# Performance work log

Hardware: AMD Instinct MI355X
Metric: run time of the kernel (lower is better)

## Reference

```python
import jax, jax.numpy as jnp
import numpy as np

B, L, D_MODEL, H, MAX_DIST = 4, 1024, 1024, 16, 64
DEPTH = D_MODEL // H
VOCAB = 2 * MAX_DIST + 1


def setup_inputs() -> dict:
    key = jax.random.key(0)
    ks = jax.random.split(key, 12)
    s = 0.02
    return {
        "x": jax.random.normal(ks[0], (B, L, D_MODEL), jnp.float32),
        "mask": jnp.zeros((B, 1, 1, L), jnp.float32),
        "wq": jax.random.normal(ks[1], (D_MODEL, D_MODEL), jnp.float32) * s,
        "bq": jnp.zeros((D_MODEL,), jnp.float32),
        "wk": jax.random.normal(ks[2], (D_MODEL, D_MODEL), jnp.float32) * s,
        "bk": jnp.zeros((D_MODEL,), jnp.float32),
        "wv": jax.random.normal(ks[3], (D_MODEL, D_MODEL), jnp.float32) * s,
        "bv": jnp.zeros((D_MODEL,), jnp.float32),
        "wo": jax.random.normal(ks[4], (D_MODEL, D_MODEL), jnp.float32) * s,
        "bo": jnp.zeros((D_MODEL,), jnp.float32),
        "rel_k_table": jax.random.normal(ks[5], (VOCAB, DEPTH), jnp.float32) * s,
        "rel_v_table": jax.random.normal(ks[6], (VOCAB, DEPTH), jnp.float32) * s,
    }


def _split_heads(t):
    # [B, L, d_model] -> [B, H, L, depth]
    return t.reshape(B, L, H, DEPTH).transpose(0, 2, 1, 3)


def reference(x, mask, wq, bq, wk, bk, wv, bv, wo, bo, rel_k_table, rel_v_table):
    # q/k/v projections (self-attention)
    q = _split_heads(x @ wq + bq)
    k = _split_heads(x @ wk + bk)
    v = _split_heads(x @ wv + bv)

    # relative positions matrix [L, L], clipped to [-MAX_DIST, MAX_DIST] then shifted
    r = jnp.arange(L)
    rel_mat = jnp.clip(r[None, :] - r[:, None], -MAX_DIST, MAX_DIST) + MAX_DIST
    rel_k = rel_k_table[rel_mat]  # [L, L, depth]
    rel_v = rel_v_table[rel_mat]  # [L, L, depth]

    # _relative_attention_inner(q, k, rel_k, transpose=True):
    # logits = q k^T + q . rel_k  (note: t2t relative path applies no 1/sqrt(dk) scale)
    logits = (jnp.einsum('bhqd,bhkd->bhqk', q, k)
              + jnp.einsum('bhqd,qkd->bhqk', q, rel_k))
    logits = logits + mask * (-1e9)  # bias
    weights = jax.nn.softmax(logits, axis=-1)  # [B, H, L, L]

    # _relative_attention_inner(weights, v, rel_v, transpose=False)
    ctx = (jnp.einsum('bhqk,bhkd->bhqd', weights, v)
           + jnp.einsum('bhqk,qkd->bhqd', weights, rel_v))

    # combine heads and output projection
    ctx = ctx.transpose(0, 2, 1, 3).reshape(B, L, D_MODEL)
    out = ctx @ wo + bo
    return out
```

## Files before the change

### kernel.cpp

```cpp
#include <hip/hip_runtime.h>
#include <hip/hip_bf16.h>
#include <cstdint>
#include <cstddef>

typedef unsigned int u32;
typedef __attribute__((ext_vector_type(8))) short s16x8;
typedef __attribute__((ext_vector_type(4))) short s16x4;
typedef __attribute__((ext_vector_type(4))) float f32x4;
typedef __attribute__((ext_vector_type(2))) u32   u32x2;

#define MFMA(a,b,c) __builtin_amdgcn_mfma_f32_16x16x32_bf16(a,b,c,0,0,0)

#if __has_builtin(__builtin_amdgcn_mfma_f32_16x16x16bf16_1k)
#define MFMA16(a,b,c) __builtin_amdgcn_mfma_f32_16x16x16bf16_1k(a,b,c,0,0,0)
#else
static __device__ __forceinline__ f32x4 MFMA16(s16x4 a, s16x4 b, f32x4 c){
    f32x4 d;
    asm("v_mfma_f32_16x16x16_bf16 %0, %1, %2, %3"
        : "=v"(d) : "v"(a), "v"(b), "v"(c));
    return d;
}
#endif

__device__ __forceinline__ short f2bf(float f) {
    u32 u = __builtin_bit_cast(u32, f);
    u32 r = (u + 0x7fffu + ((u >> 16) & 1u)) >> 16;
    return (short)r;
}
__device__ __forceinline__ float bf2f(short s) {
    return __builtin_bit_cast(float, ((u32)(unsigned short)s) << 16);
}
__device__ __forceinline__ u32 cvtpk(float lo, float hi) {
    u32 r;
    asm("v_cvt_pk_bf16_f32 %0, %1, %2" : "=v"(r) : "v"(lo), "v"(hi));
    return r;
}
__device__ __forceinline__ void async_copy16(void* lds, const void* g) {
    __builtin_amdgcn_global_load_lds((const __attribute__((address_space(1))) u32*)g,
                                     (__attribute__((address_space(3))) u32*)lds, 16, 0, 0);
}

__global__ __launch_bounds__(256)
void prep_all(const float* __restrict__ x, short* __restrict__ xb,
              const float* __restrict__ wq, const float* __restrict__ wk,
              const float* __restrict__ wv, const float* __restrict__ wo,
              short* __restrict__ Wtqkv, short* __restrict__ Wto,
              const float* __restrict__ relk, const float* __restrict__ relv,
              short* __restrict__ relkb, short* __restrict__ relvT)
{
    __shared__ float sT[64][68];
    const int bid = blockIdx.x;
    const int tid = threadIdx.x;

    if (bid < 2048) {
        int i = (bid * 256 + tid) * 8;
        float4 a = *(const float4*)&x[i];
        float4 b = *(const float4*)&x[i + 4];
        s16x8 v = { f2bf(a.x), f2bf(a.y), f2bf(a.z), f2bf(a.w),
                    f2bf(b.x), f2bf(b.y), f2bf(b.z), f2bf(b.w) };
        *(s16x8*)&xb[i] = v;
    } else if (bid < 3072) {
        const int wid = bid - 2048;
        const int kt = wid & 15, nt = (wid >> 4) & 15, seg = wid >> 8;
        const float* src = seg == 0 ? wq : seg == 1 ? wk : seg == 2 ? wv : wo;
        const int k0 = kt * 64, n0 = nt * 64;
#pragma unroll
        for (int i = 0; i < 4; ++i) {
            int t2 = tid + i * 256;
            int r = t2 >> 4, c4 = t2 & 15;
            *(float4*)&sT[r][c4 * 4] = *(const float4*)&src[(size_t)(k0 + r) * 1024 + n0 + c4 * 4];
        }
        __syncthreads();
#pragma unroll
        for (int i = 0; i < 2; ++i) {
            int t2 = tid + i * 256;
            int rn = t2 >> 3, ch = t2 & 7;
            s16x8 v;
#pragma unroll
            for (int j = 0; j < 8; ++j) v[j] = f2bf(sT[ch * 8 + j][rn]);
            if (seg < 3)
                *(s16x8*)&Wtqkv[(size_t)(seg * 1024 + n0 + rn) * 1024 + k0 + ch * 8] = v;
            else
                *(s16x8*)&Wto[(size_t)(n0 + rn) * 1024 + k0 + ch * 8] = v;
        }
    } else {
        int gt = (bid - 3072) * 256 + tid;
        for (int i = gt; i < 144 * 64; i += 256 * 8) {
            int r = i >> 6, d = i & 63;
            relkb[i] = (r < 129) ? f2bf(relk[r * 64 + d]) : (short)0;
        }
        for (int i = gt; i < 64 * 128; i += 256 * 8) {
            int d = i >> 7, r = i & 127;
            relvT[i] = f2bf(relv[r * 64 + d]);
        }
    }
}

__global__ __launch_bounds__(256, 4)
void gemm_qkv(const short* __restrict__ Ab, const short* __restrict__ Wt,
              const float* __restrict__ bq, const float* __restrict__ bk,
              const float* __restrict__ bv,
              short* __restrict__ Qb, short* __restrict__ Kb, short* __restrict__ Vtb)
{
    __shared__ __align__(16) short As[128 * 64];
    __shared__ __align__(16) short Bs[128 * 64];
    const int tid = threadIdx.x;
    const int w = tid >> 6, lane = tid & 63;
    const int lo16 = lane & 15, hi = lane >> 4;
    const int pb = blockIdx.x;
    const int wg = (pb & 7) * 96 + (pb >> 3);
    const int n0g = (wg % 24) * 128;
    const int m0 = (wg / 24) * 128;
    const int wr = w >> 1, wc = w & 1;

    f32x4 acc[4][4] = {};

    for (int t = 0; t < 16; ++t) {
        const int k0 = t * 64;
        __syncthreads();
#pragma unroll
        for (int i = 0; i < 4; ++i) {
            int o = i * 4096 + tid * 16;
            int row = o >> 7;
            int cb = o & 127;
            int sc = cb ^ ((row & 7) << 4);
            async_copy16((char*)As + o, Ab + (size_t)(m0 + row) * 1024 + k0 + (sc >> 1));
            async_copy16((char*)Bs + o, Wt + (size_t)(n0g + row) * 1024 + k0 + (sc >> 1));
        }
        __syncthreads();
#pragma unroll
        for (int ks = 0; ks < 2; ++ks) {
            s16x8 aF[4], bF[4];
#pragma unroll
            for (int mi = 0; mi < 4; ++mi) {
                int row = wr * 64 + mi * 16 + lo16;
                int cb = ks * 64 + hi * 16;
                aF[mi] = *(const s16x8*)((const char*)As + row * 128 + (cb ^ ((row & 7) << 4)));
            }
#pragma unroll
            for (int ni = 0; ni < 4; ++ni) {
                int row = wc * 64 + ni * 16 + lo16;
                int cb = ks * 64 + hi * 16;
                bF[ni] = *(const s16x8*)((const char*)Bs + row * 128 + (cb ^ ((row & 7) << 4)));
            }
#pragma unroll
            for (int mi = 0; mi < 4; ++mi)
#pragma unroll
                for (int ni = 0; ni < 4; ++ni)
                    acc[mi][ni] = MFMA(aF[mi], bF[ni], acc[mi][ni]);
        }
    }

    const int seg = n0g >> 10;
    const int nn = n0g & 1023;
    const float* bias = seg == 0 ? bq : seg == 1 ? bk : bv;
    float bv4[4];
#pragma unroll
    for (int ni = 0; ni < 4; ++ni) bv4[ni] = bias[nn + wc * 64 + ni * 16 + lo16];

    if (seg == 2) {
#pragma unroll
        for (int mi = 0; mi < 4; ++mi)
#pragma unroll
            for (int ni = 0; ni < 4; ++ni) {
                int nl = nn + wc * 64 + ni * 16 + lo16;
                int hh = nl >> 6, d = nl & 63;
                int mbase = m0 + wr * 64 + mi * 16 + hi * 4;
                int bb = mbase >> 10, l0 = mbase & 1023;
                int j0 = l0 & 31;
                int col = (l0 >> 5) * 32 + (((j0 >> 4) & 1) << 2) + (((j0 >> 2) & 3) << 3);
                s16x4 pk = { f2bf(acc[mi][ni][0] + bv4[ni]),
                             f2bf(acc[mi][ni][1] + bv4[ni]),
                             f2bf(acc[mi][ni][2] + bv4[ni]),
                             f2bf(acc[mi][ni][3] + bv4[ni]) };
                *(s16x4*)&Vtb[((size_t)(bb * 16 + hh) * 64 + d) * 1024 + col] = pk;
            }
    } else {
        short* out = seg == 0 ? Qb : Kb;
#pragma unroll
        for (int mi = 0; mi < 4; ++mi)
#pragma unroll
            for (int ni = 0; ni < 4; ++ni) {
                int nl = nn + wc * 64 + ni * 16 + lo16;
                int hh = nl >> 6, d = nl & 63;
#pragma unroll
                for (int r = 0; r < 4; ++r) {
                    int m = m0 + wr * 64 + mi * 16 + hi * 4 + r;
                    int bb = m >> 10, l = m & 1023;
                    out[(((size_t)bb * 16 + hh) * 1024 + l) * 64 + d] = f2bf(acc[mi][ni][r] + bv4[ni]);
                }
            }
    }
}

struct TileRegs {
    s16x8 k0, k1, k2, k3;
    s16x8 v0, v1, v2, v3;
    s16x4 m0, m1;
};

__device__ __forceinline__ void prefetch_tile(
    const short* __restrict__ sKc, const short* __restrict__ sVc,
    const short* __restrict__ sMaskP, int kfm, int lo16, int hi, TileRegs& R)
{
    const int km = lo16 & 7;
    R.k0 = *(const s16x8*)(sKc + lo16 * 64 + ((hi ^ km) << 3));
    R.k1 = *(const s16x8*)(sKc + lo16 * 64 + (((hi + 4) ^ km) << 3));
    R.k2 = *(const s16x8*)(sKc + (lo16 + 16) * 64 + ((hi ^ km) << 3));
    R.k3 = *(const s16x8*)(sKc + (lo16 + 16) * 64 + (((hi + 4) ^ km) << 3));
    R.v0 = *(const s16x8*)(sVc + lo16 * 32 + hi * 8);
    R.v1 = *(const s16x8*)(sVc + (16 + lo16) * 32 + hi * 8);
    R.v2 = *(const s16x8*)(sVc + (32 + lo16) * 32 + hi * 8);
    R.v3 = *(const s16x8*)(sVc + (48 + lo16) * 32 + hi * 8);
    R.m0 = *(const s16x4*)&sMaskP[kfm + hi * 4];
    R.m1 = *(const s16x4*)&sMaskP[kfm + 16 + hi * 4];
}

__device__ __forceinline__ void process32(
    int kf, int q0, int q_abs, int lo16, int hi,
    const TileRegs& R,
    const s16x8& qB0, const s16x8& qB1,
    float qrel_lo, float qrel_hi,
    const short (*sQrelw)[144], short (*sBandw)[128],
    f32x4* ctx, float& lsum, float& lov, float& hiv)
{
    const f32x4 z = {0.f, 0.f, 0.f, 0.f};
    __builtin_amdgcn_s_setprio(1);
    f32x4 sa = MFMA(R.k0, qB0, z);
    f32x4 sb = MFMA(R.k1, qB1, z);
    f32x4 sc = MFMA(R.k2, qB0, z);
    f32x4 sd = MFMA(R.k3, qB1, z);
    __builtin_amdgcn_s_setprio(0);
    f32x4 s0 = sa + sb, s1 = sc + sd;

    float p[8];
    if (kf + 95 <= q0 || kf >= q0 + 79) {
        const float qc = (kf < q0) ? qrel_lo : qrel_hi;
        float bs = 0.f;
#pragma unroll
        for (int r = 0; r < 4; ++r) {
            p[r]     = __expf(s0[r] + qc + bf2f(R.m0[r]));
            p[4 + r] = __expf(s1[r] + qc + bf2f(R.m1[r]));
        }
#pragma unroll
        for (int r = 0; r < 8; ++r) bs += p[r];
        lsum += bs;
        if (kf < q0) lov += bs; else hiv += bs;
    } else {
#pragma unroll
        for (int f = 0; f < 2; ++f)
#pragma unroll
            for (int r = 0; r < 4; ++r) {
                int k_abs = kf + f * 16 + hi * 4 + r;
                int dd = k_abs - q_abs;
                dd = dd < -64 ? -64 : (dd > 64 ? 64 : dd);
                int rel = dd + 64;
                float sv = f ? s1[r] : s0[r];
                float mv = bf2f(f ? R.m1[r] : R.m0[r]);
                float pex = __expf(sv + bf2f(sQrelw[lo16][rel]) + mv);
                p[f * 4 + r] = pex;
                lsum += pex;
                if (rel >= 1 && rel <= 127) sBandw[lo16][rel] = f2bf(pex);
                else if (rel == 0) lov += pex;
                else hiv += pex;
            }
    }

    u32x2 w0 = { cvtpk(p[0], p[1]), cvtpk(p[2], p[3]) };
    u32x2 w1 = { cvtpk(p[4], p[5]), cvtpk(p[6], p[7]) };
    s16x4 pf0 = __builtin_bit_cast(s16x4, w0);
    s16x4 pf1 = __builtin_bit_cast(s16x4, w1);

    s16x4 a0 = __builtin_shufflevector(R.v0, R.v0, 0, 1, 2, 3);
    s16x4 b0 = __builtin_shufflevector(R.v0, R.v0, 4, 5, 6, 7);
    s16x4 a1 = __builtin_shufflevector(R.v1, R.v1, 0, 1, 2, 3);
    s16x4 b1 = __builtin_shufflevector(R.v1, R.v1, 4, 5, 6, 7);
    s16x4 a2 = __builtin_shufflevector(R.v2, R.v2, 0, 1, 2, 3);
    s16x4 b2 = __builtin_shufflevector(R.v2, R.v2, 4, 5, 6, 7);
    s16x4 a3 = __builtin_shufflevector(R.v3, R.v3, 0, 1, 2, 3);
    s16x4 b3 = __builtin_shufflevector(R.v3, R.v3, 4, 5, 6, 7);

    __builtin_amdgcn_s_setprio(1);
    ctx[0] = MFMA16(a0, pf0, ctx[0]);
    ctx[1] = MFMA16(a1, pf0, ctx[1]);
    ctx[2] = MFMA16(a2, pf0, ctx[2]);
    ctx[3] = MFMA16(a3, pf0, ctx[3]);
    ctx[0] = MFMA16(b0, pf1, ctx[0]);
    ctx[1] = MFMA16(b1, pf1, ctx[1]);
    ctx[2] = MFMA16(b2, pf1, ctx[2]);
    ctx[3] = MFMA16(b3, pf1, ctx[3]);
    __builtin_amdgcn_s_setprio(0);
}

__global__ __launch_bounds__(256, 3)
void attn_mfma(const short* __restrict__ Qb, const short* __restrict__ Kb,
               const short* __restrict__ Vtb, const short* __restrict__ relkb,
               const short* __restrict__ relvTb, const float* __restrict__ relv_f32,
               const float* __restrict__ mask, short* __restrict__ CTXb)
{
    __shared__ __align__(16) short sK[2][32 * 64];
    __shared__ __align__(16) short sV[2][64 * 32];
    __shared__ __align__(16) short sMaskP[1024 + 32];
    __shared__ __align__(16) short sQrel[4][16][144];
    __shared__ __align__(16) short sBand[4][16][128];

    const int tid = threadIdx.x;
    const int w = tid >> 6, lane = tid & 63;
    const int lo16 = lane & 15, hi = lane >> 4;

    const int p = blockIdx.x;
    const int bid = (p & 7) * 128 + (p >> 3);
    const int bh = bid >> 4;
    const int qt = bid & 15;
    const int b = bh >> 4, h = bh & 15;
    const int q0 = qt * 64 + w * 16;
    const int q_abs = q0 + lo16;

    const short* Kbase = Kb + (size_t)bh * 65536;
    const short* Vtbase = Vtb + (size_t)bh * 65536;

    const int skr = tid >> 3, skc = tid & 7;
    const int svd = tid >> 2, svc = tid & 3;
    const short* ksrc = Kbase + (size_t)skr * 64 + ((skc ^ (skr & 7)) << 3);
    const short* vsrc = Vtbase + (size_t)svd * 1024 + svc * 8;

    async_copy16((char*)&sK[0][0] + tid * 16, ksrc);
    async_copy16((char*)&sK[1][0] + tid * 16, ksrc + 32 * 64);
    async_copy16((char*)&sV[0][0] + tid * 16, vsrc);
    async_copy16((char*)&sV[1][0] + tid * 16, vsrc + 32);

    const short* qptr = Qb + ((size_t)bh * 1024 + q_abs) * 64 + hi * 8;
    const s16x8 qB0 = *(const s16x8*)qptr;
    const s16x8 qB1 = *(const s16x8*)(qptr + 32);

    {
        float4 mv = *(const float4*)&mask[b * 1024 + tid * 4];
        s16x4 mp = { f2bf(mv.x * -1e9f), f2bf(mv.y * -1e9f),
                     f2bf(mv.z * -1e9f), f2bf(mv.w * -1e9f) };
        *(s16x4*)&sMaskP[tid * 4] = mp;
        if (tid < 8) *(s16x4*)&sMaskP[1024 + tid * 4] = s16x4{0, 0, 0, 0};
    }
    {
        u32* bz = (u32*)&sBand[w][0][0];
#pragma unroll
        for (int i = 0; i < 16; ++i) bz[lane + i * 64] = 0u;
    }

#pragma unroll
    for (int rf = 0; rf < 9; ++rf) {
        const short* rp = relkb + (size_t)(rf * 16 + lo16) * 64 + hi * 8;
        s16x8 rA0 = *(const s16x8*)rp;
        s16x8 rA1 = *(const s16x8*)(rp + 32);
        f32x4 dq = {0.f, 0.f, 0.f, 0.f};
        dq = MFMA(rA0, qB0, dq);
        dq = MFMA(rA1, qB1, dq);
        s16x4 pk = { f2bf(dq[0]), f2bf(dq[1]), f2bf(dq[2]), f2bf(dq[3]) };
        *(s16x4*)&sQrel[w][lo16][rf * 16 + hi * 4] = pk;
    }
    __syncthreads();

    const float qrel_lo = bf2f(sQrel[w][lo16][0]);
    const float qrel_hi = bf2f(sQrel[w][lo16][128]);

    f32x4 ctx[4] = {};
    float lsum = 0.f, lov = 0.f, hiv = 0.f;

    TileRegs R0, R1;
    for (int t = 0; t < 16; ++t) {
        prefetch_tile(sK[0], sV[0], sMaskP, t * 64,      lo16, hi, R0);
        prefetch_tile(sK[1], sV[1], sMaskP, t * 64 + 32, lo16, hi, R1);
        __syncthreads();
        const int kb = ((t + 1) & 15) * 64;
        async_copy16((char*)&sK[0][0] + tid * 16, ksrc + (size_t)kb * 64);
        async_copy16((char*)&sK[1][0] + tid * 16, ksrc + (size_t)(kb + 32) * 64);
        async_copy16((char*)&sV[0][0] + tid * 16, vsrc + kb);
        async_copy16((char*)&sV[1][0] + tid * 16, vsrc + kb + 32);
        process32(t * 64,      q0, q_abs, lo16, hi, R0, qB0, qB1, qrel_lo, qrel_hi,
                  sQrel[w], sBand[w], ctx, lsum, lov, hiv);
        process32(t * 64 + 32, q0, q_abs, lo16, hi, R1, qB0, qB1, qrel_lo, qrel_hi,
                  sQrel[w], sBand[w], ctx, lsum, lov, hiv);
        __syncthreads();
    }

#pragma unroll
    for (int ks = 0; ks < 4; ++ks) {
        s16x8 bB = *(const s16x8*)&sBand[w][lo16][ks * 32 + hi * 8];
#pragma unroll
        for (int df = 0; df < 4; ++df) {
            s16x8 rA = *(const s16x8*)(relvTb + (size_t)(df * 16 + lo16) * 128 + ks * 32 + hi * 8);
            ctx[df] = MFMA(rA, bB, ctx[df]);
        }
    }

    lsum += __shfl_xor(lsum, 16); lsum += __shfl_xor(lsum, 32);
    lov  += __shfl_xor(lov, 16);  lov  += __shfl_xor(lov, 32);
    hiv  += __shfl_xor(hiv, 16);  hiv  += __shfl_xor(hiv, 32);
    const float inv = 1.0f / lsum;

#pragma unroll
    for (int df = 0; df < 4; ++df) {
        s16x4 pk;
#pragma unroll
        for (int r = 0; r < 4; ++r) {
            int d = df * 16 + hi * 4 + r;
            float t = ctx[df][r] + lov * relv_f32[d] + hiv * relv_f32[128 * 64 + d];
            pk[r] = f2bf(t * inv);
        }
        *(s16x4*)(CTXb + ((size_t)(b * 1024) + q_abs) * 1024 + h * 64 + df * 16 + hi * 4) = pk;
    }
}

__global__ __launch_bounds__(256, 4)
void gemm_out(const short* __restrict__ Ab, const short* __restrict__ Wto,
              const float* __restrict__ bo, float* __restrict__ out)
{
    __shared__ __align__(16) short As[128 * 64];
    __shared__ __align__(16) short Bs[64 * 64];
    const int tid = threadIdx.x;
    const int w = tid >> 6, lane = tid & 63;
    const int lo16 = lane & 15, hi = lane >> 4;
    const int pb = blockIdx.x;
    const int wg = (pb & 7) * 64 + (pb >> 3);
    const int n0 = (wg & 15) * 64;
    const int m0 = (wg >> 4) * 128;
    const int wr = w;

    f32x4 acc[2][4] = {};

    for (int t = 0; t < 16; ++t) {
        const int k0 = t * 64;
        __syncthreads();
#pragma unroll
        for (int i = 0; i < 4; ++i) {
            int o = i * 4096 + tid * 16;
            int row = o >> 7;
            int cb = o & 127;
            int sc = cb ^ ((row & 7) << 4);
            async_copy16((char*)As + o, Ab + (size_t)(m0 + row) * 1024 + k0 + (sc >> 1));
        }
#pragma unroll
        for (int i = 0; i < 2; ++i) {
            int o = i * 4096 + tid * 16;
            int row = o >> 7;
            int cb = o & 127;
            int sc = cb ^ ((row & 7) << 4);
            async_copy16((char*)Bs + o, Wto + (size_t)(n0 + row) * 1024 + k0 + (sc >> 1));
        }
        __syncthreads();
#pragma unroll
        for (int ks = 0; ks < 2; ++ks) {
            s16x8 aF[2], bF[4];
#pragma unroll
            for (int mi = 0; mi < 2; ++mi) {
                int row = wr * 32 + mi * 16 + lo16;
                int cb = ks * 64 + hi * 16;
                aF[mi] = *(const s16x8*)((const char*)As + row * 128 + (cb ^ ((row & 7) << 4)));
            }
#pragma unroll
            for (int ni = 0; ni < 4; ++ni) {
                int row = ni * 16 + lo16;
                int cb = ks * 64 + hi * 16;
                bF[ni] = *(const s16x8*)((const char*)Bs + row * 128 + (cb ^ ((row & 7) << 4)));
            }
#pragma unroll
            for (int mi = 0; mi < 2; ++mi)
#pragma unroll
                for (int ni = 0; ni < 4; ++ni)
                    acc[mi][ni] = MFMA(aF[mi], bF[ni], acc[mi][ni]);
        }
    }

    float bv4[4];
#pragma unroll
    for (int ni = 0; ni < 4; ++ni) bv4[ni] = bo[n0 + ni * 16 + lo16];
#pragma unroll
    for (int mi = 0; mi < 2; ++mi)
#pragma unroll
        for (int ni = 0; ni < 4; ++ni)
#pragma unroll
            for (int r = 0; r < 4; ++r) {
                int m = m0 + wr * 32 + mi * 16 + hi * 4 + r;
                out[(size_t)m * 1024 + n0 + ni * 16 + lo16] = acc[mi][ni][r] + bv4[ni];
            }
}

extern "C" void kernel_launch(void* const* d_in, const int* in_sizes, int n_in,
                              void* d_out, int out_size, void* d_ws, size_t ws_size,
                              hipStream_t stream)
{
    (void)in_sizes; (void)n_in; (void)out_size; (void)ws_size;
    const float* x    = (const float*)d_in[0];
    const float* mask = (const float*)d_in[1];
    const float* wq   = (const float*)d_in[2];
    const float* bq   = (const float*)d_in[3];
    const float* wk   = (const float*)d_in[4];
    const float* bk   = (const float*)d_in[5];
    const float* wv   = (const float*)d_in[6];
    const float* bv   = (const float*)d_in[7];
    const float* wo   = (const float*)d_in[8];
    const float* bo   = (const float*)d_in[9];
    const float* relk = (const float*)d_in[10];
    const float* relv = (const float*)d_in[11];
    float* out = (float*)d_out;

    char* p = (char*)d_ws;
    short* xb    = (short*)p; p += (size_t)4096 * 1024 * 2;
    short* Wtqkv = (short*)p; p += (size_t)3072 * 1024 * 2;
    short* Wto   = (short*)p; p += (size_t)1024 * 1024 * 2;
    short* Qb    = (short*)p; p += (size_t)4096 * 1024 * 2;
    short* Kb    = (short*)p; p += (size_t)4096 * 1024 * 2;
    short* Vtb   = (short*)p; p += (size_t)4096 * 1024 * 2;
    short* CTXb  = (short*)p; p += (size_t)4096 * 1024 * 2;
    short* relkb = (short*)p; p += (size_t)144 * 64 * 2;
    short* relvT = (short*)p; p += (size_t)64 * 128 * 2;

    prep_all  <<<3080, 256, 0, stream>>>(x, xb, wq, wk, wv, wo, Wtqkv, Wto,
                                         relk, relv, relkb, relvT);
    gemm_qkv  <<<768, 256, 0, stream>>>(xb, Wtqkv, bq, bk, bv, Qb, Kb, Vtb);
    attn_mfma <<<1024, 256, 0, stream>>>(Qb, Kb, Vtb, relkb, relvT, relv, mask, CTXb);
    gemm_out  <<<512, 256, 0, stream>>>(CTXb, Wto, bo, out);
}
```

Baseline: 117.9 us.

## Shrink attention LDS footprint and tile to raise occupancy to four blocks

```diff
diff --git a/kernel.cpp b/kernel.cpp
--- a/kernel.cpp
+++ b/kernel.cpp
@@ -46,7 +46,8 @@
               const float* __restrict__ wv, const float* __restrict__ wo,
               short* __restrict__ Wtqkv, short* __restrict__ Wto,
               const float* __restrict__ relk, const float* __restrict__ relv,
-              short* __restrict__ relkb, short* __restrict__ relvT)
+              short* __restrict__ relkb, short* __restrict__ relvT,
+              const float* __restrict__ mask, short* __restrict__ maskPb)
 {
     __shared__ float sT[64][68];
     const int bid = blockIdx.x;
@@ -93,6 +94,8 @@
             int d = i >> 7, r = i & 127;
             relvT[i] = f2bf(relv[r * 64 + d]);
         }
+        for (int i = gt; i < 4096; i += 256 * 8)
+            maskPb[i] = f2bf(mask[i] * -1e9f);
     }
 }
 
@@ -193,115 +196,15 @@
     }
 }
 
-struct TileRegs {
-    s16x8 k0, k1, k2, k3;
-    s16x8 v0, v1, v2, v3;
-    s16x4 m0, m1;
-};
-
-__device__ __forceinline__ void prefetch_tile(
-    const short* __restrict__ sKc, const short* __restrict__ sVc,
-    const short* __restrict__ sMaskP, int kfm, int lo16, int hi, TileRegs& R)
-{
-    const int km = lo16 & 7;
-    R.k0 = *(const s16x8*)(sKc + lo16 * 64 + ((hi ^ km) << 3));
-    R.k1 = *(const s16x8*)(sKc + lo16 * 64 + (((hi + 4) ^ km) << 3));
-    R.k2 = *(const s16x8*)(sKc + (lo16 + 16) * 64 + ((hi ^ km) << 3));
-    R.k3 = *(const s16x8*)(sKc + (lo16 + 16) * 64 + (((hi + 4) ^ km) << 3));
-    R.v0 = *(const s16x8*)(sVc + lo16 * 32 + hi * 8);
-    R.v1 = *(const s16x8*)(sVc + (16 + lo16) * 32 + hi * 8);
-    R.v2 = *(const s16x8*)(sVc + (32 + lo16) * 32 + hi * 8);
-    R.v3 = *(const s16x8*)(sVc + (48 + lo16) * 32 + hi * 8);
-    R.m0 = *(const s16x4*)&sMaskP[kfm + hi * 4];
-    R.m1 = *(const s16x4*)&sMaskP[kfm + 16 + hi * 4];
-}
-
-__device__ __forceinline__ void process32(
-    int kf, int q0, int q_abs, int lo16, int hi,
-    const TileRegs& R,
-    const s16x8& qB0, const s16x8& qB1,
-    float qrel_lo, float qrel_hi,
-    const short (*sQrelw)[144], short (*sBandw)[128],
-    f32x4* ctx, float& lsum, float& lov, float& hiv)
-{
-    const f32x4 z = {0.f, 0.f, 0.f, 0.f};
-    __builtin_amdgcn_s_setprio(1);
-    f32x4 sa = MFMA(R.k0, qB0, z);
-    f32x4 sb = MFMA(R.k1, qB1, z);
-    f32x4 sc = MFMA(R.k2, qB0, z);
-    f32x4 sd = MFMA(R.k3, qB1, z);
-    __builtin_amdgcn_s_setprio(0);
-    f32x4 s0 = sa + sb, s1 = sc + sd;
-
-    float p[8];
-    if (kf + 95 <= q0 || kf >= q0 + 79) {
-        const float qc = (kf < q0) ? qrel_lo : qrel_hi;
-        float bs = 0.f;
-#pragma unroll
-        for (int r = 0; r < 4; ++r) {
-            p[r]     = __expf(s0[r] + qc + bf2f(R.m0[r]));
-            p[4 + r] = __expf(s1[r] + qc + bf2f(R.m1[r]));
-        }
-#pragma unroll
-        for (int r = 0; r < 8; ++r) bs += p[r];
-        lsum += bs;
-        if (kf < q0) lov += bs; else hiv += bs;
-    } else {
-#pragma unroll
-        for (int f = 0; f < 2; ++f)
-#pragma unroll
-            for (int r = 0; r < 4; ++r) {
-                int k_abs = kf + f * 16 + hi * 4 + r;
-                int dd = k_abs - q_abs;
-                dd = dd < -64 ? -64 : (dd > 64 ? 64 : dd);
-                int rel = dd + 64;
-                float sv = f ? s1[r] : s0[r];
-                float mv = bf2f(f ? R.m1[r] : R.m0[r]);
-                float pex = __expf(sv + bf2f(sQrelw[lo16][rel]) + mv);
-                p[f * 4 + r] = pex;
-                lsum += pex;
-                if (rel >= 1 && rel <= 127) sBandw[lo16][rel] = f2bf(pex);
-                else if (rel == 0) lov += pex;
-                else hiv += pex;
-            }
-    }
-
-    u32x2 w0 = { cvtpk(p[0], p[1]), cvtpk(p[2], p[3]) };
-    u32x2 w1 = { cvtpk(p[4], p[5]), cvtpk(p[6], p[7]) };
-    s16x4 pf0 = __builtin_bit_cast(s16x4, w0);
-    s16x4 pf1 = __builtin_bit_cast(s16x4, w1);
-
-    s16x4 a0 = __builtin_shufflevector(R.v0, R.v0, 0, 1, 2, 3);
-    s16x4 b0 = __builtin_shufflevector(R.v0, R.v0, 4, 5, 6, 7);
-    s16x4 a1 = __builtin_shufflevector(R.v1, R.v1, 0, 1, 2, 3);
-    s16x4 b1 = __builtin_shufflevector(R.v1, R.v1, 4, 5, 6, 7);
-    s16x4 a2 = __builtin_shufflevector(R.v2, R.v2, 0, 1, 2, 3);
-    s16x4 b2 = __builtin_shufflevector(R.v2, R.v2, 4, 5, 6, 7);
-    s16x4 a3 = __builtin_shufflevector(R.v3, R.v3, 0, 1, 2, 3);
-    s16x4 b3 = __builtin_shufflevector(R.v3, R.v3, 4, 5, 6, 7);
-
-    __builtin_amdgcn_s_setprio(1);
-    ctx[0] = MFMA16(a0, pf0, ctx[0]);
-    ctx[1] = MFMA16(a1, pf0, ctx[1]);
-    ctx[2] = MFMA16(a2, pf0, ctx[2]);
-    ctx[3] = MFMA16(a3, pf0, ctx[3]);
-    ctx[0] = MFMA16(b0, pf1, ctx[0]);
-    ctx[1] = MFMA16(b1, pf1, ctx[1]);
-    ctx[2] = MFMA16(b2, pf1, ctx[2]);
-    ctx[3] = MFMA16(b3, pf1, ctx[3]);
-    __builtin_amdgcn_s_setprio(0);
-}
-
-__global__ __launch_bounds__(256, 3)
+__global__ __launch_bounds__(256, 4)
 void attn_mfma(const short* __restrict__ Qb, const short* __restrict__ Kb,
                const short* __restrict__ Vtb, const short* __restrict__ relkb,
                const short* __restrict__ relvTb, const float* __restrict__ relv_f32,
-               const float* __restrict__ mask, short* __restrict__ CTXb)
+               const short* __restrict__ maskPb, short* __restrict__ CTXb)
 {
-    __shared__ __align__(16) short sK[2][32 * 64];
-    __shared__ __align__(16) short sV[2][64 * 32];
-    __shared__ __align__(16) short sMaskP[1024 + 32];
-    __shared__ __align__(16) short sQrel[4][16][144];
+    __shared__ __align__(16) short sK[32 * 64];
+    __shared__ __align__(16) short sV[64 * 32];
+    __shared__ __align__(16) short sQrel[4][16][128];
     __shared__ __align__(16) short sBand[4][16][128];
 
     const int tid = threadIdx.x;
@@ -318,34 +221,27 @@
 
     const short* Kbase = Kb + (size_t)bh * 65536;
     const short* Vtbase = Vtb + (size_t)bh * 65536;
+    const short* mbase = maskPb + b * 1024;
 
     const int skr = tid >> 3, skc = tid & 7;
     const int svd = tid >> 2, svc = tid & 3;
     const short* ksrc = Kbase + (size_t)skr * 64 + ((skc ^ (skr & 7)) << 3);
     const short* vsrc = Vtbase + (size_t)svd * 1024 + svc * 8;
 
-    async_copy16((char*)&sK[0][0] + tid * 16, ksrc);
-    async_copy16((char*)&sK[1][0] + tid * 16, ksrc + 32 * 64);
-    async_copy16((char*)&sV[0][0] + tid * 16, vsrc);
-    async_copy16((char*)&sV[1][0] + tid * 16, vsrc + 32);
+    async_copy16((char*)&sK[0] + tid * 16, ksrc);
+    async_copy16((char*)&sV[0] + tid * 16, vsrc);
 
     const short* qptr = Qb + ((size_t)bh * 1024 + q_abs) * 64 + hi * 8;
     const s16x8 qB0 = *(const s16x8*)qptr;
     const s16x8 qB1 = *(const s16x8*)(qptr + 32);
 
     {
-        float4 mv = *(const float4*)&mask[b * 1024 + tid * 4];
-        s16x4 mp = { f2bf(mv.x * -1e9f), f2bf(mv.y * -1e9f),
-                     f2bf(mv.z * -1e9f), f2bf(mv.w * -1e9f) };
-        *(s16x4*)&sMaskP[tid * 4] = mp;
-        if (tid < 8) *(s16x4*)&sMaskP[1024 + tid * 4] = s16x4{0, 0, 0, 0};
-    }
-    {
         u32* bz = (u32*)&sBand[w][0][0];
 #pragma unroll
         for (int i = 0; i < 16; ++i) bz[lane + i * 64] = 0u;
     }
 
+    f32x4 dq8 = {0.f, 0.f, 0.f, 0.f};
 #pragma unroll
     for (int rf = 0; rf < 9; ++rf) {
         const short* rp = relkb + (size_t)(rf * 16 + lo16) * 64 + hi * 8;
@@ -354,31 +250,106 @@
         f32x4 dq = {0.f, 0.f, 0.f, 0.f};
         dq = MFMA(rA0, qB0, dq);
         dq = MFMA(rA1, qB1, dq);
-        s16x4 pk = { f2bf(dq[0]), f2bf(dq[1]), f2bf(dq[2]), f2bf(dq[3]) };
-        *(s16x4*)&sQrel[w][lo16][rf * 16 + hi * 4] = pk;
-    }
+        if (rf < 8) {
+            s16x4 pk = { f2bf(dq[0]), f2bf(dq[1]), f2bf(dq[2]), f2bf(dq[3]) };
+            *(s16x4*)&sQrel[w][lo16][rf * 16 + hi * 4] = pk;
+        } else {
+            dq8 = dq;
+        }
+    }
+    const float qrel_lo = bf2f(sQrel[w][lo16][0]);
+    const float qrel_hi = __shfl(f2bf(dq8[0]) != 0 ? bf2f(f2bf(dq8[0])) : 0.0f, lo16);
+
     __syncthreads();
-
-    const float qrel_lo = bf2f(sQrel[w][lo16][0]);
-    const float qrel_hi = bf2f(sQrel[w][lo16][128]);
 
     f32x4 ctx[4] = {};
     float lsum = 0.f, lov = 0.f, hiv = 0.f;
-
-    TileRegs R0, R1;
-    for (int t = 0; t < 16; ++t) {
-        prefetch_tile(sK[0], sV[0], sMaskP, t * 64,      lo16, hi, R0);
-        prefetch_tile(sK[1], sV[1], sMaskP, t * 64 + 32, lo16, hi, R1);
-        __syncthreads();
-        const int kb = ((t + 1) & 15) * 64;
-        async_copy16((char*)&sK[0][0] + tid * 16, ksrc + (size_t)kb * 64);
-        async_copy16((char*)&sK[1][0] + tid * 16, ksrc + (size_t)(kb + 32) * 64);
-        async_copy16((char*)&sV[0][0] + tid * 16, vsrc + kb);
-        async_copy16((char*)&sV[1][0] + tid * 16, vsrc + kb + 32);
-        process32(t * 64,      q0, q_abs, lo16, hi, R0, qB0, qB1, qrel_lo, qrel_hi,
-                  sQrel[w], sBand[w], ctx, lsum, lov, hiv);
-        process32(t * 64 + 32, q0, q_abs, lo16, hi, R1, qB0, qB1, qrel_lo, qrel_hi,
-                  sQrel[w], sBand[w], ctx, lsum, lov, hiv);
+    const f32x4 z = {0.f, 0.f, 0.f, 0.f};
+    const int km = lo16 & 7;
+
+    for (int t = 0; t < 32; ++t) {
+        const int kf = t * 32;
+        s16x8 kr0 = *(const s16x8*)(sK + lo16 * 64 + ((hi ^ km) << 3));
+        s16x8 kr1 = *(const s16x8*)(sK + lo16 * 64 + (((hi + 4) ^ km) << 3));
+        s16x8 kr2 = *(const s16x8*)(sK + (lo16 + 16) * 64 + ((hi ^ km) << 3));
+        s16x8 kr3 = *(const s16x8*)(sK + (lo16 + 16) * 64 + (((hi + 4) ^ km) << 3));
+        s16x8 vr0 = *(const s16x8*)(sV + lo16 * 32 + hi * 8);
+        s16x8 vr1 = *(const s16x8*)(sV + (16 + lo16) * 32 + hi * 8);
+        s16x8 vr2 = *(const s16x8*)(sV + (32 + lo16) * 32 + hi * 8);
+        s16x8 vr3 = *(const s16x8*)(sV + (48 + lo16) * 32 + hi * 8);
+        s16x4 m0 = *(const s16x4*)&mbase[kf + hi * 4];
+        s16x4 m1 = *(const s16x4*)&mbase[kf + 16 + hi * 4];
+        __syncthreads();
+        const int kfn = ((t + 1) & 31) * 32;
+        async_copy16((char*)&sK[0] + tid * 16, ksrc + (size_t)kfn * 64);
+        async_copy16((char*)&sV[0] + tid * 16, vsrc + kfn);
+
+        __builtin_amdgcn_s_setprio(1);
+        f32x4 s0 = MFMA(kr0, qB0, z);
+        f32x4 s1 = MFMA(kr2, qB0, z);
+        s0 = MFMA(kr1, qB1, s0);
+        s1 = MFMA(kr3, qB1, s1);
+        __builtin_amdgcn_s_setprio(0);
+
+        float pr[8];
+        if (kf + 95 <= q0 || kf >= q0 + 79) {
+            const float qc = (kf < q0) ? qrel_lo : qrel_hi;
+            float bs = 0.f;
+#pragma unroll
+            for (int r = 0; r < 4; ++r) {
+                pr[r]     = __expf(s0[r] + qc + bf2f(m0[r]));
+                pr[4 + r] = __expf(s1[r] + qc + bf2f(m1[r]));
+            }
+#pragma unroll
+            for (int r = 0; r < 8; ++r) bs += pr[r];
+            lsum += bs;
+            if (kf < q0) lov += bs; else hiv += bs;
+        } else {
+#pragma unroll
+            for (int f = 0; f < 2; ++f)
+#pragma unroll
+                for (int r = 0; r < 4; ++r) {
+                    int k_abs = kf + f * 16 + hi * 4 + r;
+                    int dd = k_abs - q_abs;
+                    dd = dd < -64 ? -64 : (dd > 64 ? 64 : dd);
+                    int rel = dd + 64;
+                    int relc = rel > 127 ? 127 : rel;
+                    float qv = bf2f(sQrel[w][lo16][relc]);
+                    if (rel == 128) qv = qrel_hi;
+                    float sv = f ? s1[r] : s0[r];
+                    float mv = bf2f(f ? m1[r] : m0[r]);
+                    float pex = __expf(sv + qv + mv);
+                    pr[f * 4 + r] = pex;
+                    lsum += pex;
+                    if (rel >= 1 && rel <= 127) sBand[w][lo16][rel] = f2bf(pex);
+                    else if (rel == 0) lov += pex;
+                    else hiv += pex;
+                }
+        }
+        u32x2 w0 = { cvtpk(pr[0], pr[1]), cvtpk(pr[2], pr[3]) };
+        u32x2 w1 = { cvtpk(pr[4], pr[5]), cvtpk(pr[6], pr[7]) };
+        s16x4 pf0 = __builtin_bit_cast(s16x4, w0);
+        s16x4 pf1 = __builtin_bit_cast(s16x4, w1);
+
+        s16x4 a0 = __builtin_shufflevector(vr0, vr0, 0, 1, 2, 3);
+        s16x4 b0 = __builtin_shufflevector(vr0, vr0, 4, 5, 6, 7);
+        s16x4 a1 = __builtin_shufflevector(vr1, vr1, 0, 1, 2, 3);
+        s16x4 b1 = __builtin_shufflevector(vr1, vr1, 4, 5, 6, 7);
+        s16x4 a2 = __builtin_shufflevector(vr2, vr2, 0, 1, 2, 3);
+        s16x4 b2 = __builtin_shufflevector(vr2, vr2, 4, 5, 6, 7);
+        s16x4 a3 = __builtin_shufflevector(vr3, vr3, 0, 1, 2, 3);
+        s16x4 b3 = __builtin_shufflevector(vr3, vr3, 4, 5, 6, 7);
+        __builtin_amdgcn_s_setprio(1);
+        ctx[0] = MFMA16(a0, pf0, ctx[0]);
+        ctx[1] = MFMA16(a1, pf0, ctx[1]);
+        ctx[2] = MFMA16(a2, pf0, ctx[2]);
+        ctx[3] = MFMA16(a3, pf0, ctx[3]);
+        ctx[0] = MFMA16(b0, pf1, ctx[0]);
+        ctx[1] = MFMA16(b1, pf1, ctx[1]);
+        ctx[2] = MFMA16(b2, pf1, ctx[2]);
+        ctx[3] = MFMA16(b3, pf1, ctx[3]);
+        __builtin_amdgcn_s_setprio(0);
+
         __syncthreads();
     }
 
@@ -504,19 +475,20 @@
     float* out = (float*)d_out;
 
     char* p = (char*)d_ws;
-    short* xb    = (short*)p; p += (size_t)4096 * 1024 * 2;
-    short* Wtqkv = (short*)p; p += (size_t)3072 * 1024 * 2;
-    short* Wto   = (short*)p; p += (size_t)1024 * 1024 * 2;
-    short* Qb    = (short*)p; p += (size_t)4096 * 1024 * 2;
-    short* Kb    = (short*)p; p += (size_t)4096 * 1024 * 2;
-    short* Vtb   = (short*)p; p += (size_t)4096 * 1024 * 2;
-    short* CTXb  = (short*)p; p += (size_t)4096 * 1024 * 2;
-    short* relkb = (short*)p; p += (size_t)144 * 64 * 2;
-    short* relvT = (short*)p; p += (size_t)64 * 128 * 2;
+    short* xb     = (short*)p; p += (size_t)4096 * 1024 * 2;
+    short* Wtqkv  = (short*)p; p += (size_t)3072 * 1024 * 2;
+    short* Wto    = (short*)p; p += (size_t)1024 * 1024 * 2;
+    short* Qb     = (short*)p; p += (size_t)4096 * 1024 * 2;
+    short* Kb     = (short*)p; p += (size_t)4096 * 1024 * 2;
+    short* Vtb    = (short*)p; p += (size_t)4096 * 1024 * 2;
+    short* CTXb   = (short*)p; p += (size_t)4096 * 1024 * 2;
+    short* relkb  = (short*)p; p += (size_t)144 * 64 * 2;
+    short* relvT  = (short*)p; p += (size_t)64 * 128 * 2;
+    short* maskPb = (short*)p; p += (size_t)4096 * 2;
 
     prep_all  <<<3080, 256, 0, stream>>>(x, xb, wq, wk, wv, wo, Wtqkv, Wto,
-                                         relk, relv, relkb, relvT);
+                                         relk, relv, relkb, relvT, mask, maskPb);
     gemm_qkv  <<<768, 256, 0, stream>>>(xb, Wtqkv, bq, bk, bv, Qb, Kb, Vtb);
-    attn_mfma <<<1024, 256, 0, stream>>>(Qb, Kb, Vtb, relkb, relvT, relv, mask, CTXb);
+    attn_mfma <<<1024, 256, 0, stream>>>(Qb, Kb, Vtb, relkb, relvT, relv, maskPb, CTXb);
     gemm_out  <<<512, 256, 0, stream>>>(CTXb, Wto, bo, out);
 }
```

After: 114.4 us. 2.9% less time.
